# Performance work log

Hardware: AMD Instinct MI355X
Metric: run time of the kernel (lower is better)

The kernel has to match this reference:

```python
import jax, jax.numpy as jnp
import numpy as np

IN_CH = 256
OUT_CH = 256
LATENT = 512
SCALE = 1.0 / IN_CH ** 0.5


def setup_inputs() -> dict:
    key = jax.random.key(0)
    k1, k2, k3, k4 = jax.random.split(key, 4)
    return {
        "x": jax.random.normal(k1, (16, IN_CH, 64, 64), dtype=jnp.float32),
        "w": jax.random.normal(k2, (16, LATENT), dtype=jnp.float32),
        "style_w": jax.random.normal(k3, (IN_CH, LATENT), dtype=jnp.float32) * (1.0 / LATENT ** 0.5),
        "style_b": jnp.zeros((IN_CH,), dtype=jnp.float32),
        "weight": jax.random.normal(k4, (1, OUT_CH, IN_CH, 3, 3), dtype=jnp.float32),
    }


def reference(x, w, style_w, style_b, weight):
    b, c, h, ws = x.shape
    # style = Linear(latent -> in_channels), reshaped to [b,1,in,1,1]
    style = (w @ style_w.T + style_b)[:, None, :, None, None]
    wt = weight * SCALE                    # [1, O, I, 3, 3]
    wt = wt * (style + 1.0)                # [b, O, I, 3, 3]
    demod = jax.lax.rsqrt(jnp.sum(wt * wt, axis=(2, 3, 4), keepdims=True) + 1e-8)
    wt = wt * demod
    # grouped conv: fold batch into channels, groups = b
    x2 = x.reshape(1, b * c, h, ws)
    k = wt.reshape(b * OUT_CH, c, 3, 3)
    out = jax.lax.conv_general_dilated(
        x2, k,
        window_strides=(1, 1),
        padding=((1, 1), (1, 1)),
        dimension_numbers=("NCHW", "OIHW", "NCHW"),
        feature_group_count=b,
    )
    return out.reshape(b, OUT_CH, h, ws)
```

## Files before the change

### kernel.cpp

```cpp
#include <hip/hip_runtime.h>
#include <hip/hip_bf16.h>

#define IN_CH 256
#define OUT_CH 256
#define LATENT 512
#define MSCALE (1.0f / 16.0f)

typedef __attribute__((ext_vector_type(8)))  short bf16x8;
typedef __attribute__((ext_vector_type(16))) float f32x16;
typedef unsigned short u16;
typedef unsigned int u32;

__device__ __forceinline__ u16 f2bf(float f) {
  unsigned int x = __float_as_uint(f);
  x += 0x7fffu + ((x >> 16) & 1u);
  return (u16)(x >> 16);
}

__device__ __forceinline__ u32 pkbf(float lo, float hi) {
  u32 r;
  asm("v_cvt_pk_bf16_f32 %0, %1, %2" : "=v"(r) : "v"(lo), "v"(hi));
  return r;
}

__device__ __forceinline__ void gload_lds16(const u16* g, u16* l) {
#if defined(__has_builtin) && __has_builtin(__builtin_amdgcn_global_load_lds)
  __builtin_amdgcn_global_load_lds(
      (const __attribute__((address_space(1))) unsigned int*)g,
      (__attribute__((address_space(3))) unsigned int*)l, 16, 0, 0);
#else
  int lane = __builtin_amdgcn_mbcnt_hi(~0u, __builtin_amdgcn_mbcnt_lo(~0u, 0));
  ((uint4*)l)[lane] = *(const uint4*)g;
#endif
}

__global__ void k_prep(const float* __restrict__ weight, const float* __restrict__ w,
                       const float* __restrict__ sw, const float* __restrict__ sb,
                       float* __restrict__ wsq, u16* __restrict__ wb,
                       float* __restrict__ mod) {
  const int bid = blockIdx.x, tid = threadIdx.x;
  if (bid < 256) {
    const int o = bid, i = tid;
    const float* wp = weight + ((size_t)o * IN_CH + i) * 9;
    float s = 0.f;
#pragma unroll
    for (int t = 0; t < 9; ++t) {
      float v = wp[t];
      s += v * v;
      wb[(((size_t)t * 32 + (i >> 3)) * OUT_CH + o) * 8 + (i & 7)] = f2bf(v);
    }
    wsq[o * IN_CH + i] = s;
  } else {
    __shared__ float ws[LATENT];
    const int b = bid - 256;
    ws[tid] = w[b * LATENT + tid];
    ws[tid + 256] = w[b * LATENT + 256 + tid];
    __syncthreads();
    const float4* sr = (const float4*)(sw + (size_t)tid * LATENT);
    const float4* wr = (const float4*)ws;
    float s = 0.f;
#pragma unroll 8
    for (int l = 0; l < LATENT / 4; ++l) {
      float4 a = sr[l], c = wr[l];
      s += a.x * c.x + a.y * c.y + a.z * c.z + a.w * c.w;
    }
    mod[b * IN_CH + tid] = (1.0f + s + sb[tid]) * MSCALE;
  }
}

__global__ __launch_bounds__(256, 2)
void k_conv(const float* __restrict__ x, const u16* __restrict__ wb,
            const float* __restrict__ mod, const float* __restrict__ wsq,
            float* __restrict__ out) {
  __shared__ __align__(16) u16 xlds[2 * 10 * 2 * 66 * 8];
  __shared__ __align__(16) u16 wlds[2 * 9 * 2 * 64 * 8];
  __shared__ __align__(16) float modsh[IN_CH];
  __shared__ __align__(16) float dmsh[64];

  const int tid = threadIdx.x;
  const int lane = tid & 63;
  const int wid = tid >> 6;
  const int ol = lane & 31;
  const int hi = lane >> 5;

  const int bid = blockIdx.x;
  const int sbid = ((bid & 7) << 6) | (bid >> 3);
  const int otile = (sbid & 3) << 6;
  const int hbase = ((sbid >> 2) & 7) << 3;
  const int b = sbid >> 5;

  const int sg = (tid >> 6) & 1;
  const int sc1 = tid & 63;
  const int rhalf = tid >> 7;
  const float* xb = x + (size_t)b * 1048576 + sg * 8 * 4096 + sc1;

  int woff[4];
#pragma unroll
  for (int it = 0; it < 4; ++it) {
    int p = it * 256 + tid;
    int t = p >> 7, g = (p >> 6) & 1, o = p & 63;
    woff[it] = ((t * 32 + g) * OUT_CH + otile + o) * 8;
  }
  const int wofft = ((8 * 32 + ((tid >> 6) & 1)) * OUT_CH + otile + (tid & 63)) * 8;

  float va[5][8];
  float mvv[8];
  auto ldmod = [&](int ib) {
    float4 m0 = *(const float4*)(modsh + ib + sg * 8);
    float4 m1 = *(const float4*)(modsh + ib + sg * 8 + 4);
    mvv[0] = m0.x; mvv[1] = m0.y; mvv[2] = m0.z; mvv[3] = m0.w;
    mvv[4] = m1.x; mvv[5] = m1.y; mvv[6] = m1.z; mvv[7] = m1.w;
  };
  auto issueX = [&](int k, int ib, float* v) {
    const int pr = hbase + 2 * k + rhalf;
    const int hc = min(max(pr - 1, 0), 63);
    const float* p = xb + hc * 64 + (size_t)ib * 4096;
#pragma unroll
    for (int j = 0; j < 8; ++j) v[j] = p[(size_t)j * 4096];
  };
  auto commitX = [&](int k, u16* xd, const float* v) {
    const int pr = hbase + 2 * k + rhalf;
    const bool vr = (pr >= 1) && (pr <= 64);
    uint4 q;
    q.x = vr ? pkbf(v[0] * mvv[0], v[1] * mvv[1]) : 0u;
    q.y = vr ? pkbf(v[2] * mvv[2], v[3] * mvv[3]) : 0u;
    q.z = vr ? pkbf(v[4] * mvv[4], v[5] * mvv[5]) : 0u;
    q.w = vr ? pkbf(v[6] * mvv[6], v[7] * mvv[7]) : 0u;
    *(uint4*)(xd + (size_t)(((2 * k + rhalf) * 2 + sg) * 66 + sc1 + 1) * 8) = q;
  };
  auto stageW = [&](int ibw, u16* wd) {
#pragma unroll
    for (int it = 0; it < 4; ++it)
      gload_lds16(wb + woff[it] + ibw, wd + (size_t)(it * 256 + wid * 64) * 8);
    if (tid < 128)
      gload_lds16(wb + wofft + ibw, wd + (size_t)(1024 + wid * 64) * 8);
  };

  f32x16 acc[2][4] = {};

  modsh[tid] = mod[b * IN_CH + tid];
  if (tid < 80) {
    const int q = tid;
    const int bufz = q / 40, rem = q - bufz * 40;
    const int r = rem >> 2, g = (rem >> 1) & 1, ce = (rem & 1) * 65;
    bf16x8 z = {};
    *(bf16x8*)(xlds + (size_t)(bufz * 1320 + (r * 2 + g) * 66 + ce) * 8) = z;
  }
#pragma unroll
  for (int k = 0; k < 5; ++k) issueX(k, 0, va[k]);
  stageW(0, wlds);
  __syncthreads();

  if (tid < 64) {
    const int o = otile + tid;
    const float4* wr = (const float4*)(wsq + (size_t)o * IN_CH);
    const float4* mq = (const float4*)modsh;
    float s = 1e-8f;
#pragma unroll 4
    for (int i = 0; i < IN_CH / 4; ++i) {
      float4 a = wr[i], c = mq[i];
      s += a.x * (c.x * c.x) + a.y * (c.y * c.y) + a.z * (c.z * c.z) + a.w * (c.w * c.w);
    }
    dmsh[tid] = rsqrtf(s);
  }
  ldmod(0);
#pragma unroll
  for (int k = 0; k < 5; ++k) commitX(k, xlds, va[k]);
  __syncthreads();

  for (int ic = 0; ic < 16; ++ic) {
    const int buf = ic & 1;
    const u16* xp = xlds + buf * 10560;
    const u16* wp = wlds + buf * 9216;
    u16* xd = xlds + (buf ^ 1) * 10560;
    u16* wd = wlds + (buf ^ 1) * 9216;
    const bool pf = (ic < 15);
    const int ib = (ic + 1) << 4;

    if (pf) {
      ldmod(ib);
#pragma unroll
      for (int k = 0; k < 5; ++k) issueX(k, ib, va[k]);
      stageW((ic + 1) * 4096, wd);
    }

    __builtin_amdgcn_s_setprio(1);
#pragma unroll
    for (int dh = 0; dh < 3; ++dh) {
#pragma unroll
      for (int dw = 0; dw < 3; ++dw) {
        const int t = dh * 3 + dw;
        bf16x8 A0 = *(const bf16x8*)(wp + (size_t)((t * 2 + hi) * 64 + ol) * 8);
        bf16x8 A1 = *(const bf16x8*)(wp + (size_t)((t * 2 + hi) * 64 + 32 + ol) * 8);
#pragma unroll
        for (int ps = 0; ps < 4; ++ps) {
          const int r = 2 * wid + (ps >> 1) + dh;
          const int c = (ps & 1) * 32 + ol + dw;
          bf16x8 B = *(const bf16x8*)(xp + (size_t)((r * 2 + hi) * 66 + c) * 8);
          acc[0][ps] = __builtin_amdgcn_mfma_f32_32x32x16_bf16(A0, B, acc[0][ps], 0, 0, 0);
          acc[1][ps] = __builtin_amdgcn_mfma_f32_32x32x16_bf16(A1, B, acc[1][ps], 0, 0, 0);
        }
      }
    }
    __builtin_amdgcn_s_setprio(0);

    if (pf) {
#pragma unroll
      for (int k = 0; k < 5; ++k) commitX(k, xd, va[k]);
    }
    __syncthreads();
  }

  float* outb = out + (size_t)b * OUT_CH * 4096;
#pragma unroll
  for (int os = 0; os < 2; ++os) {
    float dm[16];
#pragma unroll
    for (int qd = 0; qd < 4; ++qd) {
      float4 d4 = *(const float4*)(dmsh + os * 32 + qd * 8 + hi * 4);
      dm[qd * 4 + 0] = d4.x; dm[qd * 4 + 1] = d4.y;
      dm[qd * 4 + 2] = d4.z; dm[qd * 4 + 3] = d4.w;
    }
#pragma unroll
    for (int ps = 0; ps < 4; ++ps) {
      const int prow = hbase + 2 * wid + (ps >> 1);
      const int col = (ps & 1) * 32 + ol;
#pragma unroll
      for (int rr = 0; rr < 16; ++rr) {
        const int orow = (rr & 3) + 8 * (rr >> 2) + 4 * hi;
        const int o = otile + os * 32 + orow;
        outb[(size_t)o * 4096 + prow * 64 + col] = acc[os][ps][rr] * dm[rr];
      }
    }
  }
}

extern "C" void kernel_launch(void* const* d_in, const int* in_sizes, int n_in,
                              void* d_out, int out_size, void* d_ws, size_t ws_size,
                              hipStream_t stream) {
  const float* x  = (const float*)d_in[0];
  const float* w  = (const float*)d_in[1];
  const float* sw = (const float*)d_in[2];
  const float* sb = (const float*)d_in[3];
  const float* wt = (const float*)d_in[4];
  float* out = (float*)d_out;

  char* ws = (char*)d_ws;
  u16*   wbuf  = (u16*)(ws);
  float* mod   = (float*)(ws + 1179648);
  float* wsq   = (float*)(ws + 1196032);
  if (ws_size < 1458176u) return;

  k_prep<<<272, 256, 0, stream>>>(wt, w, sw, sb, wsq, wbuf, mod);
  k_conv<<<512, 256, 0, stream>>>(x, wbuf, mod, wsq, out);
}
```

Before: 102.2 us.

## Stage x rows in three batches interleaved with MFMA loops using float2 loads

Changes how the input tile is loaded. Each thread now reads pairs of adjacent columns with float2 loads and handles one row per batch, so the 10 rows go out in three smaller batches. Those batches are issued and committed to LDS between the three dh iterations of the MFMA loop, instead of all being issued up front and committed after the whole loop. The aim is to cut register pressure from holding five rows of prefetched values and to spread the global-load latency across the compute. The trade-off is that the loads are in flight for a shorter time before they are needed, and the priority toggles add more scheduling points.

```diff
diff --git a/kernel.cpp b/kernel.cpp
--- a/kernel.cpp
+++ b/kernel.cpp
@@ -89,10 +89,10 @@
   const int hbase = ((sbid >> 2) & 7) << 3;
   const int b = sbid >> 5;
 
-  const int sg = (tid >> 6) & 1;
-  const int sc1 = tid & 63;
-  const int rhalf = tid >> 7;
-  const float* xb = x + (size_t)b * 1048576 + sg * 8 * 4096 + sc1;
+  const int rbase = tid >> 6;
+  const int g2 = (tid >> 5) & 1;
+  const int c2 = tid & 31;
+  const float* xb2 = x + (size_t)b * 1048576 + (size_t)g2 * 8 * 4096 + 2 * c2;
 
   int woff[4];
 #pragma unroll
@@ -103,30 +103,38 @@
   }
   const int wofft = ((8 * 32 + ((tid >> 6) & 1)) * OUT_CH + otile + (tid & 63)) * 8;
 
-  float va[5][8];
   float mvv[8];
   auto ldmod = [&](int ib) {
-    float4 m0 = *(const float4*)(modsh + ib + sg * 8);
-    float4 m1 = *(const float4*)(modsh + ib + sg * 8 + 4);
+    float4 m0 = *(const float4*)(modsh + ib + g2 * 8);
+    float4 m1 = *(const float4*)(modsh + ib + g2 * 8 + 4);
     mvv[0] = m0.x; mvv[1] = m0.y; mvv[2] = m0.z; mvv[3] = m0.w;
     mvv[4] = m1.x; mvv[5] = m1.y; mvv[6] = m1.z; mvv[7] = m1.w;
   };
-  auto issueX = [&](int k, int ib, float* v) {
-    const int pr = hbase + 2 * k + rhalf;
+  auto issueX = [&](int r, int iboff, float* v) {
+    const int pr = hbase + r;
     const int hc = min(max(pr - 1, 0), 63);
-    const float* p = xb + hc * 64 + (size_t)ib * 4096;
-#pragma unroll
-    for (int j = 0; j < 8; ++j) v[j] = p[(size_t)j * 4096];
-  };
-  auto commitX = [&](int k, u16* xd, const float* v) {
-    const int pr = hbase + 2 * k + rhalf;
+    const float* p = xb2 + (size_t)iboff * 4096 + hc * 64;
+#pragma unroll
+    for (int j = 0; j < 8; ++j) {
+      float2 t2 = *(const float2*)(p + (size_t)j * 4096);
+      v[2 * j] = t2.x; v[2 * j + 1] = t2.y;
+    }
+  };
+  auto commitX = [&](int r, u16* xd, const float* v) {
+    const int pr = hbase + r;
     const bool vr = (pr >= 1) && (pr <= 64);
-    uint4 q;
-    q.x = vr ? pkbf(v[0] * mvv[0], v[1] * mvv[1]) : 0u;
-    q.y = vr ? pkbf(v[2] * mvv[2], v[3] * mvv[3]) : 0u;
-    q.z = vr ? pkbf(v[4] * mvv[4], v[5] * mvv[5]) : 0u;
-    q.w = vr ? pkbf(v[6] * mvv[6], v[7] * mvv[7]) : 0u;
-    *(uint4*)(xd + (size_t)(((2 * k + rhalf) * 2 + sg) * 66 + sc1 + 1) * 8) = q;
+    uint4 qa, qb;
+    qa.x = vr ? pkbf(v[0]  * mvv[0], v[2]  * mvv[1]) : 0u;
+    qa.y = vr ? pkbf(v[4]  * mvv[2], v[6]  * mvv[3]) : 0u;
+    qa.z = vr ? pkbf(v[8]  * mvv[4], v[10] * mvv[5]) : 0u;
+    qa.w = vr ? pkbf(v[12] * mvv[6], v[14] * mvv[7]) : 0u;
+    qb.x = vr ? pkbf(v[1]  * mvv[0], v[3]  * mvv[1]) : 0u;
+    qb.y = vr ? pkbf(v[5]  * mvv[2], v[7]  * mvv[3]) : 0u;
+    qb.z = vr ? pkbf(v[9]  * mvv[4], v[11] * mvv[5]) : 0u;
+    qb.w = vr ? pkbf(v[13] * mvv[6], v[15] * mvv[7]) : 0u;
+    u16* base = xd + (size_t)((r * 2 + g2) * 66 + 1 + 2 * c2) * 8;
+    *(uint4*)base = qa;
+    *(uint4*)(base + 8) = qb;
   };
   auto stageW = [&](int ibw, u16* wd) {
 #pragma unroll
@@ -137,6 +145,7 @@
   };
 
   f32x16 acc[2][4] = {};
+  float va[16], vb[16];
 
   modsh[tid] = mod[b * IN_CH + tid];
   if (tid < 80) {
@@ -146,9 +155,8 @@
     bf16x8 z = {};
     *(bf16x8*)(xlds + (size_t)(bufz * 1320 + (r * 2 + g) * 66 + ce) * 8) = z;
   }
-#pragma unroll
-  for (int k = 0; k < 5; ++k) issueX(k, 0, va[k]);
   stageW(0, wlds);
+  issueX(rbase, 0, va);
   __syncthreads();
 
   if (tid < 64) {
@@ -164,8 +172,10 @@
     dmsh[tid] = rsqrtf(s);
   }
   ldmod(0);
-#pragma unroll
-  for (int k = 0; k < 5; ++k) commitX(k, xlds, va[k]);
+  commitX(rbase, xlds, va);
+  issueX(rbase + 4, 0, vb);
+  commitX(rbase + 4, xlds, vb);
+  if (tid < 128) { issueX(rbase + 8, 0, va); commitX(rbase + 8, xlds, va); }
   __syncthreads();
 
   for (int ic = 0; ic < 16; ++ic) {
@@ -179,14 +189,13 @@
 
     if (pf) {
       ldmod(ib);
-#pragma unroll
-      for (int k = 0; k < 5; ++k) issueX(k, ib, va[k]);
       stageW((ic + 1) * 4096, wd);
-    }
-
-    __builtin_amdgcn_s_setprio(1);
+      issueX(rbase, ib, va);
+    }
+
 #pragma unroll
     for (int dh = 0; dh < 3; ++dh) {
+      __builtin_amdgcn_s_setprio(1);
 #pragma unroll
       for (int dw = 0; dw < 3; ++dw) {
         const int t = dh * 3 + dw;
@@ -201,12 +210,18 @@
           acc[1][ps] = __builtin_amdgcn_mfma_f32_32x32x16_bf16(A1, B, acc[1][ps], 0, 0, 0);
         }
       }
-    }
-    __builtin_amdgcn_s_setprio(0);
-
-    if (pf) {
-#pragma unroll
-      for (int k = 0; k < 5; ++k) commitX(k, xd, va[k]);
+      __builtin_amdgcn_s_setprio(0);
+      if (pf) {
+        if (dh == 0) {
+          commitX(rbase, xd, va);
+          issueX(rbase + 4, ib, vb);
+        } else if (dh == 1) {
+          commitX(rbase + 4, xd, vb);
+          if (tid < 128) issueX(rbase + 8, ib, va);
+        } else {
+          if (tid < 128) commitX(rbase + 8, xd, va);
+        }
+      }
     }
     __syncthreads();
   }
```

Measured after the change: 99.33 us (median of 2 runs). 2.8% less time.
